# Optimization experiments

Hardware: AMD Instinct MI355X
Metric: run time of the kernel (lower is better)

Reference implementation:

```python
import jax, jax.numpy as jnp
import numpy as np
import math
from jax import lax

N = 5          # kernel_size (hard-coded PHT assumes 5x5)
K = N // 2     # 2
EPS = 1e-6
THETA = 0.7

def _pht_kernel_np():
    # H_i = cos(2*pi*2*r^2 + 0*theta) on the 5x5 grid, times calibrated spectral weights, plus eps
    coords = np.arange(N, dtype=np.float32) - K
    gv, gu = np.meshgrid(coords, coords, indexing='ij')  # torch.meshgrid default is 'ij'
    r2 = (gu ** 2 + gv ** 2) / (K * K + EPS)
    H = np.cos(2.0 * math.pi * 2.0 * r2).astype(np.float32)
    target = np.zeros((N, N), np.float32)
    target[K, K] = -4.0
    target[K - 1, K] = 1.0
    target[K + 1, K] = 1.0
    target[K, K - 1] = 1.0
    target[K, K + 1] = 1.0
    sw = np.where(target != 0, target / H, 0.0).astype(np.float32)
    return (H * sw + EPS).astype(np.float32)  # (5,5)

def _rotation_maps_np():
    # Replicates rotate_kernel exactly: float32 cos/sin, int() truncation, later (h,w) overwrite.
    angles = np.linspace(0, 2 * np.pi, 8, endpoint=False)
    SH = np.zeros((8, N, N), np.int32)
    SW = np.zeros((8, N, N), np.int32)
    M = np.zeros((8, N, N), np.float32)
    for ai, a in enumerate(angles):
        c = float(np.cos(np.float32(a)))
        s = float(np.sin(np.float32(a)))
        for h in range(N):
            for w in range(N):
                rh = int(h * c + w * (-s))
                rw = int(h * s + w * c)
                if 0 <= rh < N and 0 <= rw < N:
                    SH[ai, rh, rw] = h
                    SW[ai, rh, rw] = w
                    M[ai, rh, rw] = 1.0
    return SH, SW, M

_PHT = jnp.asarray(_pht_kernel_np())                     # (5,5)
_sh, _sw, _m = _rotation_maps_np()
_SH = jnp.asarray(_sh)
_SW = jnp.asarray(_sw)
_MASK = jnp.asarray(_m)

def setup_inputs() -> dict:
    key = jax.random.key(0)
    k1, k2 = jax.random.split(key)
    x = jax.random.normal(k1, (32, 64, 128, 128), dtype=jnp.float32)
    weight = jax.random.normal(k2, (64, 64, 5, 5), dtype=jnp.float32) * 0.05
    alpha = jnp.ones((1,), dtype=jnp.float32)
    return {"x": x, "weight": weight, "alpha": alpha}

def reference(x, weight, alpha):
    # Branch 1: PHT-modulated weight, averaged over 8 SO(2) rotations.
    # pht_kernel is (C_in,1,5,5) with identical values per channel -> broadcast (5,5).
    w_eff = weight * alpha[0] * _PHT[None, None]          # (Co,Ci,5,5)
    # rotated[o,i,a,rh,rw] = w_eff[o,i,SH[a,rh,rw],SW[a,rh,rw]] * MASK
    rotated = w_eff[:, :, _SH, _SW] * _MASK               # (Co,Ci,8,5,5)
    # conv is linear in weight: mean of 8 convs == conv with mean kernel
    mean_k = rotated.mean(axis=2)                         # (Co,Ci,5,5)
    out = lax.conv_general_dilated(
        x, mean_k, window_strides=(1, 1), padding=[(2, 2), (2, 2)],
        dimension_numbers=("NCHW", "OIHW", "NCHW"))
    # Branch 2: 1x1 kernel_diff; rotation of a 1x1 kernel is identity, mean of 8 == single conv.
    kd = weight.sum(axis=(2, 3))                          # (Co,Ci)
    out_diff = jnp.einsum("oi,bihw->bohw", kd, x)
    return out - THETA * out_diff
```

## Files before the change

### kernel.cpp

```cpp
#include <hip/hip_runtime.h>
#include <stdint.h>

typedef __attribute__((ext_vector_type(8))) __bf16 bf16x8;
typedef __attribute__((ext_vector_type(16))) float f32x16;
typedef __attribute__((ext_vector_type(4))) unsigned int u32x4;
typedef __attribute__((ext_vector_type(2))) float f32x2;
typedef unsigned int u32;
typedef unsigned short u16;

#define THETA 0.7f

__host__ __device__ constexpr float pht_val(int q) {
  return (q == 12) ? (-4.0f + 1e-6f)
       : (q == 7 || q == 11 || q == 13 || q == 17) ? (1.0f + 1e-6f)
       : 1e-6f;
}

__device__ __forceinline__ u16 f2bf(float v) {
  u32 u = __builtin_bit_cast(u32, v);
  return (u16)((u + 0x7fffu + ((u >> 16) & 1u)) >> 16);
}

__global__ __launch_bounds__(256) void k_prep(const float* __restrict__ wgt,
                                              const float* __restrict__ alpha,
                                              u16* __restrict__ apack) {
  int t = blockIdx.x * 256 + threadIdx.x;
  int o = t >> 6, ci = t & 63;
  const float* wp = wgt + ((size_t)(o * 64 + ci)) * 25;
  float wv[25], sumw = 0.f;
#pragma unroll
  for (int p = 0; p < 25; ++p) { wv[p] = wp[p]; sumw += wv[p]; }
  float keff[25];
#pragma unroll
  for (int p = 0; p < 25; ++p) keff[p] = pht_val(p) * wv[p];
  constexpr int TP[33] = {0,1,2,3,4,6,7,9,12,13,  0,1,2,3,4,  0, 0, 0,
                          0,5,10,15,20,  0,5,6,10,11,12,15,17,20,21};
  constexpr int TQ[33] = {5,6,12,17,23,10,16,22,20,21,  0,5,10,15,20,  5, 0, 5,
                          0,6,7,8,9,  5,6,2,12,8,4,17,9,23,14};
#pragma unroll
  for (int e = 0; e < 33; ++e) keff[TP[e]] += pht_val(TQ[e]) * wv[TQ[e]];

  float al = alpha[0];
  int kc = ci >> 4, oh = o >> 5;
  int lane = ((ci >> 3) & 1) * 32 + (o & 31);
#pragma unroll
  for (int p = 0; p < 25; ++p) {
    float v = al * (keff[p] * 0.125f);
    if (p == 12) v -= THETA * sumw;
    size_t idx = ((((size_t)p * 4 + kc) * 2 + oh) * 64 + lane) * 8 + (ci & 7);
    apack[idx] = f2bf(v);
  }
}

#define ROWB 4608

#define MM(A, B, C) __builtin_amdgcn_mfma_f32_32x32x16_bf16((A), __builtin_bit_cast(bf16x8, (B)), (C), 0, 0, 0)

#define LDBR(S, DX, KC) do {                                                \
    const char* pb_ = pcol + (DX) * 128;                                    \
    int gx_ = ((((KC) * 2 + lhi) ^ ((l31 + (DX)) & 7)) << 4);               \
    br##S##0 = *(const u32x4*)(pb_ + 0 * ROWB + gx_);                       \
    br##S##1 = *(const u32x4*)(pb_ + 1 * ROWB + gx_);                       \
    br##S##2 = *(const u32x4*)(pb_ + 2 * ROWB + gx_);                       \
    br##S##3 = *(const u32x4*)(pb_ + 3 * ROWB + gx_);                       \
    br##S##4 = *(const u32x4*)(pb_ + 4 * ROWB + gx_);                       \
    br##S##5 = *(const u32x4*)(pb_ + 5 * ROWB + gx_);                       \
    br##S##6 = *(const u32x4*)(pb_ + 6 * ROWB + gx_);                       \
    br##S##7 = *(const u32x4*)(pb_ + 7 * ROWB + gx_);                       \
  } while (0)

#define LDAF(S, DX, KC) do {                                                \
    af##S##0 = apb[(size_t)((0 * 5 + (DX)) * 512 + (KC) * 128)];            \
    af##S##1 = apb[(size_t)((1 * 5 + (DX)) * 512 + (KC) * 128)];            \
    af##S##2 = apb[(size_t)((2 * 5 + (DX)) * 512 + (KC) * 128)];            \
    af##S##3 = apb[(size_t)((3 * 5 + (DX)) * 512 + (KC) * 128)];            \
    af##S##4 = apb[(size_t)((4 * 5 + (DX)) * 512 + (KC) * 128)];            \
  } while (0)

#define BURST(S) do {                                                       \
    bf16x8 A_;                                                              \
    A_ = __builtin_bit_cast(bf16x8, af##S##0);                              \
    a0 = MM(A_, br##S##0, a0); a1 = MM(A_, br##S##1, a1);                   \
    a2 = MM(A_, br##S##2, a2); a3 = MM(A_, br##S##3, a3);                   \
    A_ = __builtin_bit_cast(bf16x8, af##S##1);                              \
    a0 = MM(A_, br##S##1, a0); a1 = MM(A_, br##S##2, a1);                   \
    a2 = MM(A_, br##S##3, a2); a3 = MM(A_, br##S##4, a3);                   \
    A_ = __builtin_bit_cast(bf16x8, af##S##2);                              \
    a0 = MM(A_, br##S##2, a0); a1 = MM(A_, br##S##3, a1);                   \
    a2 = MM(A_, br##S##4, a2); a3 = MM(A_, br##S##5, a3);                   \
    A_ = __builtin_bit_cast(bf16x8, af##S##3);                              \
    a0 = MM(A_, br##S##3, a0); a1 = MM(A_, br##S##4, a1);                   \
    a2 = MM(A_, br##S##5, a2); a3 = MM(A_, br##S##6, a3);                   \
    A_ = __builtin_bit_cast(bf16x8, af##S##4);                              \
    a0 = MM(A_, br##S##4, a0); a1 = MM(A_, br##S##5, a1);                   \
    a2 = MM(A_, br##S##6, a2); a3 = MM(A_, br##S##7, a3);                   \
  } while (0)

#define SGB __builtin_amdgcn_sched_group_barrier
#define SCHED_FULL() do {                                                   \
    SGB(0x020, 5, 0);                           \
    SGB(0x100, 2, 0); SGB(0x008, 5, 0);                                     \
    SGB(0x100, 2, 0); SGB(0x008, 5, 0);                                     \
    SGB(0x100, 2, 0); SGB(0x008, 5, 0);                                     \
    SGB(0x100, 2, 0); SGB(0x008, 5, 0);                                     \
  } while (0)

#define ITER(CUR, NXT, DXN, KCN) do {                                       \
    LDBR(NXT, DXN, KCN); LDAF(NXT, DXN, KCN); BURST(CUR); SCHED_FULL();     \
  } while (0)

#define STAGE_SLOT(CP, GG) do {                                             \
    int pxb_ = px0 + 2 * (CP) - 2;                                          \
    bool ok_ = rowok && ((unsigned)pxb_ < 128u);                            \
    const float* ps_ = xr + (size_t)(8 * (GG)) * 16384 + pxb_;              \
    f32x2 v0 = {0.f, 0.f}, v1 = {0.f, 0.f}, v2 = {0.f, 0.f}, v3 = {0.f, 0.f}; \
    f32x2 v4 = {0.f, 0.f}, v5 = {0.f, 0.f}, v6 = {0.f, 0.f}, v7 = {0.f, 0.f}; \
    if (ok_) {                                                              \
      v0 = *(const f32x2*)(ps_);                                            \
      v1 = *(const f32x2*)(ps_ + 16384);                                    \
      v2 = *(const f32x2*)(ps_ + 2 * 16384);                                \
      v3 = *(const f32x2*)(ps_ + 3 * 16384);                                \
      v4 = *(const f32x2*)(ps_ + 4 * 16384);                                \
      v5 = *(const f32x2*)(ps_ + 5 * 16384);                                \
      v6 = *(const f32x2*)(ps_ + 6 * 16384);                                \
      v7 = *(const f32x2*)(ps_ + 7 * 16384);                                \
    }                                                                       \
    u32x4 wx_, wy_;                                                         \
    wx_[0] = (u32)f2bf(v0.x) | ((u32)f2bf(v1.x) << 16);                     \
    wx_[1] = (u32)f2bf(v2.x) | ((u32)f2bf(v3.x) << 16);                     \
    wx_[2] = (u32)f2bf(v4.x) | ((u32)f2bf(v5.x) << 16);                     \
    wx_[3] = (u32)f2bf(v6.x) | ((u32)f2bf(v7.x) << 16);                     \
    wy_[0] = (u32)f2bf(v0.y) | ((u32)f2bf(v1.y) << 16);                     \
    wy_[1] = (u32)f2bf(v2.y) | ((u32)f2bf(v3.y) << 16);                     \
    wy_[2] = (u32)f2bf(v4.y) | ((u32)f2bf(v5.y) << 16);                     \
    wy_[3] = (u32)f2bf(v6.y) | ((u32)f2bf(v7.y) << 16);                     \
    int c0_ = 2 * (CP);                                                     \
    *(u32x4*)(rowbase + c0_ * 128 + (((GG) ^ (c0_ & 7)) << 4)) = wx_;       \
    *(u32x4*)(rowbase + (c0_ + 1) * 128 + (((GG) ^ ((c0_ + 1) & 7)) << 4)) = wy_; \
  } while (0)

__global__ __launch_bounds__(128, 2) void k_conv(const float* __restrict__ x,
                                                 const u32x4* __restrict__ apv,
                                                 float* __restrict__ out) {
  __shared__ char tile[8 * ROWB];
  int bid = blockIdx.x;
  int lg = (bid & 7) * 512 + (bid >> 3);
  int pxq = lg & 3, yt = (lg >> 2) & 31, n = lg >> 7;
  int y0 = yt * 4, px0 = pxq * 32;
  int tid = threadIdx.x;
  int l = tid & 63;

  {
    const float* xn = x + (size_t)n * (64 * 16384);
    int sp = tid & 15, sg = tid >> 4;
    int hp = 16 + (tid >> 3), hg = tid & 7;
#pragma unroll
    for (int rr = 0; rr < 8; ++rr) {
      int sy = y0 + rr - 2;
      bool rowok = (unsigned)sy < 128u;
      char* rowbase = tile + rr * ROWB;
      const float* xr = xn + (size_t)sy * 128;
      STAGE_SLOT(sp, sg);
      if (tid < 16) STAGE_SLOT(hp, hg);
    }
  }

  int oh = tid >> 6;
  int l31 = l & 31, lhi = l >> 5;
  const u32x4* apb = apv + (size_t)(oh * 64 + l);
  const char* pcol = tile + l31 * 128;

  u32x4 brA0, brA1, brA2, brA3, brA4, brA5, brA6, brA7;
  u32x4 brB0, brB1, brB2, brB3, brB4, brB5, brB6, brB7;
  u32x4 afA0, afA1, afA2, afA3, afA4;
  u32x4 afB0, afB1, afB2, afB3, afB4;

  LDAF(A, 0, 0);
  __syncthreads();
  LDBR(A, 0, 0);

  f32x16 a0 = 0, a1 = 0, a2 = 0, a3 = 0;

  ITER(A, B, 0, 1);
  ITER(B, A, 0, 2);
  ITER(A, B, 0, 3);
  ITER(B, A, 1, 0);
  ITER(A, B, 1, 1);
  ITER(B, A, 1, 2);
  ITER(A, B, 1, 3);
  ITER(B, A, 2, 0);
  ITER(A, B, 2, 1);
  ITER(B, A, 2, 2);
  ITER(A, B, 2, 3);
  ITER(B, A, 3, 0);
  ITER(A, B, 3, 1);
  ITER(B, A, 3, 2);
  ITER(A, B, 3, 3);
  ITER(B, A, 4, 0);
  ITER(A, B, 4, 1);
  ITER(B, A, 4, 2);
  ITER(A, B, 4, 3);
  BURST(B);

  float* ob = out + ((size_t)(n * 64 + oh * 32) * 128 + y0) * 128
              + px0 + l31;
#pragma unroll
  for (int rg = 0; rg < 16; ++rg) {
    int orow = (rg & 3) + 8 * (rg >> 2) + 4 * lhi;
    float* obr = ob + (size_t)orow * 16384;
    obr[0]   = a0[rg];
    obr[128] = a1[rg];
    obr[256] = a2[rg];
    obr[384] = a3[rg];
  }
}

extern "C" void kernel_launch(void* const* d_in, const int* in_sizes, int n_in,
                              void* d_out, int out_size, void* d_ws, size_t ws_size,
                              hipStream_t stream) {
  const float* x     = (const float*)d_in[0];
  const float* wgt   = (const float*)d_in[1];
  const float* alpha = (const float*)d_in[2];
  float* out = (float*)d_out;

  u16* apack = (u16*)d_ws;

  k_prep<<<16,   256, 0, stream>>>(wgt, alpha, apack);
  k_conv<<<4096, 128, 0, stream>>>(x, (const u32x4*)apack, out);
}
```

Measured before the change: 131.4 us.

## Process four row tiles per block with a ring buffer and overlapped staging

Each block now computes 16 output rows, in four 4-row steps, instead of 4, so the grid shrinks from 4096 blocks to 1024. A 12-slot ring buffer in LDS holds input rows, and the global loads and bf16 conversion for the next 4 rows are interleaved with the current step's MFMA bursts. This reuses the overlapping halo rows between steps and hides the load latency. Row stride is padded to 4624 bytes. It costs more LDS (about 55KB per block), more registers for the staged values, and fewer blocks, which may hurt occupancy and load balance.

```diff
diff --git a/kernel.cpp b/kernel.cpp
--- a/kernel.cpp
+++ b/kernel.cpp
@@ -52,21 +52,21 @@
   }
 }
 
-#define ROWB 4608
+#define ROWB 4624
+#define NSLOT 12
 
 #define MM(A, B, C) __builtin_amdgcn_mfma_f32_32x32x16_bf16((A), __builtin_bit_cast(bf16x8, (B)), (C), 0, 0, 0)
 
 #define LDBR(S, DX, KC) do {                                                \
-    const char* pb_ = pcol + (DX) * 128;                                    \
     int gx_ = ((((KC) * 2 + lhi) ^ ((l31 + (DX)) & 7)) << 4);               \
-    br##S##0 = *(const u32x4*)(pb_ + 0 * ROWB + gx_);                       \
-    br##S##1 = *(const u32x4*)(pb_ + 1 * ROWB + gx_);                       \
-    br##S##2 = *(const u32x4*)(pb_ + 2 * ROWB + gx_);                       \
-    br##S##3 = *(const u32x4*)(pb_ + 3 * ROWB + gx_);                       \
-    br##S##4 = *(const u32x4*)(pb_ + 4 * ROWB + gx_);                       \
-    br##S##5 = *(const u32x4*)(pb_ + 5 * ROWB + gx_);                       \
-    br##S##6 = *(const u32x4*)(pb_ + 6 * ROWB + gx_);                       \
-    br##S##7 = *(const u32x4*)(pb_ + 7 * ROWB + gx_);                       \
+    br##S##0 = *(const u32x4*)(rb0 + (DX) * 128 + gx_);                     \
+    br##S##1 = *(const u32x4*)(rb1 + (DX) * 128 + gx_);                     \
+    br##S##2 = *(const u32x4*)(rb2 + (DX) * 128 + gx_);                     \
+    br##S##3 = *(const u32x4*)(rb3 + (DX) * 128 + gx_);                     \
+    br##S##4 = *(const u32x4*)(rb4 + (DX) * 128 + gx_);                     \
+    br##S##5 = *(const u32x4*)(rb5 + (DX) * 128 + gx_);                     \
+    br##S##6 = *(const u32x4*)(rb6 + (DX) * 128 + gx_);                     \
+    br##S##7 = *(const u32x4*)(rb7 + (DX) * 128 + gx_);                     \
   } while (0)
 
 #define LDAF(S, DX, KC) do {                                                \
@@ -98,7 +98,7 @@
 
 #define SGB __builtin_amdgcn_sched_group_barrier
 #define SCHED_FULL() do {                                                   \
-    SGB(0x020, 5, 0);                           \
+    SGB(0x020, 5, 0);                                                       \
     SGB(0x100, 2, 0); SGB(0x008, 5, 0);                                     \
     SGB(0x100, 2, 0); SGB(0x008, 5, 0);                                     \
     SGB(0x100, 2, 0); SGB(0x008, 5, 0);                                     \
@@ -109,109 +109,189 @@
     LDBR(NXT, DXN, KCN); LDAF(NXT, DXN, KCN); BURST(CUR); SCHED_FULL();     \
   } while (0)
 
-#define STAGE_SLOT(CP, GG) do {                                             \
-    int pxb_ = px0 + 2 * (CP) - 2;                                          \
-    bool ok_ = rowok && ((unsigned)pxb_ < 128u);                            \
-    const float* ps_ = xr + (size_t)(8 * (GG)) * 16384 + pxb_;              \
-    f32x2 v0 = {0.f, 0.f}, v1 = {0.f, 0.f}, v2 = {0.f, 0.f}, v3 = {0.f, 0.f}; \
-    f32x2 v4 = {0.f, 0.f}, v5 = {0.f, 0.f}, v6 = {0.f, 0.f}, v7 = {0.f, 0.f}; \
-    if (ok_) {                                                              \
-      v0 = *(const f32x2*)(ps_);                                            \
-      v1 = *(const f32x2*)(ps_ + 16384);                                    \
-      v2 = *(const f32x2*)(ps_ + 2 * 16384);                                \
-      v3 = *(const f32x2*)(ps_ + 3 * 16384);                                \
-      v4 = *(const f32x2*)(ps_ + 4 * 16384);                                \
-      v5 = *(const f32x2*)(ps_ + 5 * 16384);                                \
-      v6 = *(const f32x2*)(ps_ + 6 * 16384);                                \
-      v7 = *(const f32x2*)(ps_ + 7 * 16384);                                \
+#define PK(VA, VB) ((u32)f2bf(VA) | ((u32)f2bf(VB) << 16))
+
+#define SLOAD(SYE) do {                                                     \
+    int sy_ = (SYE);                                                        \
+    bool rok_ = (unsigned)sy_ < 128u;                                       \
+    const float* brr_ = xn + (size_t)sy_ * 128;                             \
+    if (rok_ && pxAok) {                                                    \
+      const float* p0_ = brr_ + (size_t)(8 * g0A) * 16384 + pxA;            \
+      const float* p1_ = brr_ + (size_t)(8 * g1A) * 16384 + pxA;            \
+      sv0 = *(const f32x2*)(p0_);               sv1 = *(const f32x2*)(p0_ + 16384);     \
+      sv2 = *(const f32x2*)(p0_ + 2 * 16384);   sv3 = *(const f32x2*)(p0_ + 3 * 16384); \
+      sv4 = *(const f32x2*)(p0_ + 4 * 16384);   sv5 = *(const f32x2*)(p0_ + 5 * 16384); \
+      sv6 = *(const f32x2*)(p0_ + 6 * 16384);   sv7 = *(const f32x2*)(p0_ + 7 * 16384); \
+      sv8 = *(const f32x2*)(p1_);               sv9 = *(const f32x2*)(p1_ + 16384);     \
+      sv10 = *(const f32x2*)(p1_ + 2 * 16384);  sv11 = *(const f32x2*)(p1_ + 3 * 16384);\
+      sv12 = *(const f32x2*)(p1_ + 4 * 16384);  sv13 = *(const f32x2*)(p1_ + 5 * 16384);\
+      sv14 = *(const f32x2*)(p1_ + 6 * 16384);  sv15 = *(const f32x2*)(p1_ + 7 * 16384);\
+    } else {                                                                \
+      sv0 = z2; sv1 = z2; sv2 = z2; sv3 = z2; sv4 = z2; sv5 = z2;           \
+      sv6 = z2; sv7 = z2; sv8 = z2; sv9 = z2; sv10 = z2; sv11 = z2;         \
+      sv12 = z2; sv13 = z2; sv14 = z2; sv15 = z2;                           \
     }                                                                       \
+    if (dutyB) {                                                            \
+      if (rok_ && pxBok) {                                                  \
+        const float* pb_ = brr_ + (size_t)(8 * gB) * 16384 + pxB;           \
+        sb0 = *(const f32x2*)(pb_);              sb1 = *(const f32x2*)(pb_ + 16384);     \
+        sb2 = *(const f32x2*)(pb_ + 2 * 16384);  sb3 = *(const f32x2*)(pb_ + 3 * 16384); \
+        sb4 = *(const f32x2*)(pb_ + 4 * 16384);  sb5 = *(const f32x2*)(pb_ + 5 * 16384); \
+        sb6 = *(const f32x2*)(pb_ + 6 * 16384);  sb7 = *(const f32x2*)(pb_ + 7 * 16384); \
+      } else {                                                              \
+        sb0 = z2; sb1 = z2; sb2 = z2; sb3 = z2;                             \
+        sb4 = z2; sb5 = z2; sb6 = z2; sb7 = z2;                             \
+      }                                                                     \
+    }                                                                       \
+  } while (0)
+
+#define SWRITE(WS) do {                                                     \
+    char* wb_ = tile + (size_t)(WS) * ROWB;                                 \
+    int c0_ = 2 * cpA;                                                      \
     u32x4 wx_, wy_;                                                         \
-    wx_[0] = (u32)f2bf(v0.x) | ((u32)f2bf(v1.x) << 16);                     \
-    wx_[1] = (u32)f2bf(v2.x) | ((u32)f2bf(v3.x) << 16);                     \
-    wx_[2] = (u32)f2bf(v4.x) | ((u32)f2bf(v5.x) << 16);                     \
-    wx_[3] = (u32)f2bf(v6.x) | ((u32)f2bf(v7.x) << 16);                     \
-    wy_[0] = (u32)f2bf(v0.y) | ((u32)f2bf(v1.y) << 16);                     \
-    wy_[1] = (u32)f2bf(v2.y) | ((u32)f2bf(v3.y) << 16);                     \
-    wy_[2] = (u32)f2bf(v4.y) | ((u32)f2bf(v5.y) << 16);                     \
-    wy_[3] = (u32)f2bf(v6.y) | ((u32)f2bf(v7.y) << 16);                     \
-    int c0_ = 2 * (CP);                                                     \
-    *(u32x4*)(rowbase + c0_ * 128 + (((GG) ^ (c0_ & 7)) << 4)) = wx_;       \
-    *(u32x4*)(rowbase + (c0_ + 1) * 128 + (((GG) ^ ((c0_ + 1) & 7)) << 4)) = wy_; \
+    wx_[0] = PK(sv0.x, sv1.x); wx_[1] = PK(sv2.x, sv3.x);                   \
+    wx_[2] = PK(sv4.x, sv5.x); wx_[3] = PK(sv6.x, sv7.x);                   \
+    wy_[0] = PK(sv0.y, sv1.y); wy_[1] = PK(sv2.y, sv3.y);                   \
+    wy_[2] = PK(sv4.y, sv5.y); wy_[3] = PK(sv6.y, sv7.y);                   \
+    *(u32x4*)(wb_ + c0_ * 128 + ((g0A ^ (c0_ & 7)) << 4)) = wx_;            \
+    *(u32x4*)(wb_ + (c0_ + 1) * 128 + ((g0A ^ ((c0_ + 1) & 7)) << 4)) = wy_;\
+    wx_[0] = PK(sv8.x, sv9.x);  wx_[1] = PK(sv10.x, sv11.x);                \
+    wx_[2] = PK(sv12.x, sv13.x); wx_[3] = PK(sv14.x, sv15.x);               \
+    wy_[0] = PK(sv8.y, sv9.y);  wy_[1] = PK(sv10.y, sv11.y);                \
+    wy_[2] = PK(sv12.y, sv13.y); wy_[3] = PK(sv14.y, sv15.y);               \
+    *(u32x4*)(wb_ + c0_ * 128 + ((g1A ^ (c0_ & 7)) << 4)) = wx_;            \
+    *(u32x4*)(wb_ + (c0_ + 1) * 128 + ((g1A ^ ((c0_ + 1) & 7)) << 4)) = wy_;\
+    if (dutyB) {                                                            \
+      int cb_ = 2 * cpB;                                                    \
+      u32x4 ux_, uy_;                                                       \
+      ux_[0] = PK(sb0.x, sb1.x); ux_[1] = PK(sb2.x, sb3.x);                 \
+      ux_[2] = PK(sb4.x, sb5.x); ux_[3] = PK(sb6.x, sb7.x);                 \
+      uy_[0] = PK(sb0.y, sb1.y); uy_[1] = PK(sb2.y, sb3.y);                 \
+      uy_[2] = PK(sb4.y, sb5.y); uy_[3] = PK(sb6.y, sb7.y);                 \
+      *(u32x4*)(wb_ + cb_ * 128 + ((gB ^ (cb_ & 7)) << 4)) = ux_;           \
+      *(u32x4*)(wb_ + (cb_ + 1) * 128 + ((gB ^ ((cb_ + 1) & 7)) << 4)) = uy_;\
+    }                                                                       \
+  } while (0)
+
+#define TBAR() do {                                                         \
+    asm volatile("s_waitcnt lgkmcnt(0)" ::: "memory");                      \
+    __builtin_amdgcn_sched_barrier(0);                                      \
+    __builtin_amdgcn_s_barrier();                                           \
+    __builtin_amdgcn_sched_barrier(0);                                      \
   } while (0)
 
 __global__ __launch_bounds__(128, 2) void k_conv(const float* __restrict__ x,
                                                  const u32x4* __restrict__ apv,
                                                  float* __restrict__ out) {
-  __shared__ char tile[8 * ROWB];
+  __shared__ char tile[NSLOT * ROWB];
   int bid = blockIdx.x;
-  int lg = (bid & 7) * 512 + (bid >> 3);
-  int pxq = lg & 3, yt = (lg >> 2) & 31, n = lg >> 7;
-  int y0 = yt * 4, px0 = pxq * 32;
+  int lg = (bid & 7) * 128 + (bid >> 3);
+  int pxq = lg & 3, yc = (lg >> 2) & 7, n = lg >> 5;
+  int px0 = pxq * 32, yb = yc * 16;
   int tid = threadIdx.x;
-  int l = tid & 63;
-
-  {
-    const float* xn = x + (size_t)n * (64 * 16384);
-    int sp = tid & 15, sg = tid >> 4;
-    int hp = 16 + (tid >> 3), hg = tid & 7;
-#pragma unroll
-    for (int rr = 0; rr < 8; ++rr) {
-      int sy = y0 + rr - 2;
-      bool rowok = (unsigned)sy < 128u;
-      char* rowbase = tile + rr * ROWB;
-      const float* xr = xn + (size_t)sy * 128;
-      STAGE_SLOT(sp, sg);
-      if (tid < 16) STAGE_SLOT(hp, hg);
-    }
-  }
-
-  int oh = tid >> 6;
+  int l = tid & 63, oh = tid >> 6;
   int l31 = l & 31, lhi = l >> 5;
+
+  int rrA = oh;
+  int m = tid & 63;
+  int cpA = m >> 2;
+  int g0A = ((m & 3) * 2 + (cpA & 1)) & 7;
+  int g1A = (g0A + 1) & 7;
+  int pxA = px0 + 2 * cpA - 2;
+  bool pxAok = pxA >= 0;
+  bool dutyB = m < 16;
+  int cpB = 16 + ((m >> 3) & 1);
+  int gB = m & 7;
+  int pxB = px0 + 2 * cpB - 2;
+  bool pxBok = (pxB + 1) < 128;
+
+  const float* xn = x + (size_t)n * (64 * 16384);
+  const f32x2 z2 = {0.f, 0.f};
+
+  f32x2 sv0, sv1, sv2, sv3, sv4, sv5, sv6, sv7;
+  f32x2 sv8, sv9, sv10, sv11, sv12, sv13, sv14, sv15;
+  f32x2 sb0, sb1, sb2, sb3, sb4, sb5, sb6, sb7;
+
+  SLOAD(yb - 2 + 0 + rrA); SWRITE(0 + rrA);
+  SLOAD(yb - 2 + 2 + rrA); SWRITE(2 + rrA);
+  SLOAD(yb - 2 + 4 + rrA); SWRITE(4 + rrA);
+  SLOAD(yb - 2 + 6 + rrA); SWRITE(6 + rrA);
+
   const u32x4* apb = apv + (size_t)(oh * 64 + l);
-  const char* pcol = tile + l31 * 128;
-
   u32x4 brA0, brA1, brA2, brA3, brA4, brA5, brA6, brA7;
   u32x4 brB0, brB1, brB2, brB3, brB4, brB5, brB6, brB7;
   u32x4 afA0, afA1, afA2, afA3, afA4;
   u32x4 afB0, afB1, afB2, afB3, afB4;
 
   LDAF(A, 0, 0);
-  __syncthreads();
-  LDBR(A, 0, 0);
+  TBAR();
 
   f32x16 a0 = 0, a1 = 0, a2 = 0, a3 = 0;
-
-  ITER(A, B, 0, 1);
-  ITER(B, A, 0, 2);
-  ITER(A, B, 0, 3);
-  ITER(B, A, 1, 0);
-  ITER(A, B, 1, 1);
-  ITER(B, A, 1, 2);
-  ITER(A, B, 1, 3);
-  ITER(B, A, 2, 0);
-  ITER(A, B, 2, 1);
-  ITER(B, A, 2, 2);
-  ITER(A, B, 2, 3);
-  ITER(B, A, 3, 0);
-  ITER(A, B, 3, 1);
-  ITER(B, A, 3, 2);
-  ITER(A, B, 3, 3);
-  ITER(B, A, 4, 0);
-  ITER(A, B, 4, 1);
-  ITER(B, A, 4, 2);
-  ITER(A, B, 4, 3);
-  BURST(B);
-
-  float* ob = out + ((size_t)(n * 64 + oh * 32) * 128 + y0) * 128
-              + px0 + l31;
-#pragma unroll
-  for (int rg = 0; rg < 16; ++rg) {
-    int orow = (rg & 3) + 8 * (rg >> 2) + 4 * lhi;
-    float* obr = ob + (size_t)orow * 16384;
-    obr[0]   = a0[rg];
-    obr[128] = a1[rg];
-    obr[256] = a2[rg];
-    obr[384] = a3[rg];
+  char* tl31 = tile + l31 * 128;
+  int b = 0;
+
+#pragma unroll 1
+  for (int t = 0; t < 4; ++t) {
+    int s4 = b + 4; if (s4 >= 12) s4 -= 12;
+    int s5 = b + 5; if (s5 >= 12) s5 -= 12;
+    int s6 = b + 6; if (s6 >= 12) s6 -= 12;
+    int s7 = b + 7; if (s7 >= 12) s7 -= 12;
+    char* rb0 = tl31 + b * ROWB;
+    char* rb1 = tl31 + (b + 1) * ROWB;
+    char* rb2 = tl31 + (b + 2) * ROWB;
+    char* rb3 = tl31 + (b + 3) * ROWB;
+    char* rb4 = tl31 + s4 * ROWB;
+    char* rb5 = tl31 + s5 * ROWB;
+    char* rb6 = tl31 + s6 * ROWB;
+    char* rb7 = tl31 + s7 * ROWB;
+
+    LDBR(A, 0, 0);
+    LDAF(A, 0, 0);
+    ITER(A, B, 0, 1);
+    ITER(B, A, 0, 2);
+    ITER(A, B, 0, 3);
+    ITER(B, A, 1, 0);
+    ITER(A, B, 1, 1);
+    ITER(B, A, 1, 2);
+    if (t < 3) SLOAD(yb + 6 + 4 * t + rrA);
+    ITER(A, B, 1, 3);
+    ITER(B, A, 2, 0);
+    ITER(A, B, 2, 1);
+    if (t < 3) {
+      int wsA = b + 8 + rrA; if (wsA >= 12) wsA -= 12;
+      SWRITE(wsA);
+    }
+    ITER(B, A, 2, 2);
+    ITER(A, B, 2, 3);
+    ITER(B, A, 3, 0);
+    ITER(A, B, 3, 1);
+    ITER(B, A, 3, 2);
+    ITER(A, B, 3, 3);
+    if (t < 3) SLOAD(yb + 8 + 4 * t + rrA);
+    ITER(B, A, 4, 0);
+    ITER(A, B, 4, 1);
+    ITER(B, A, 4, 2);
+    ITER(A, B, 4, 3);
+    BURST(B);
+    if (t < 3) {
+      int wsB = b + 10 + rrA; if (wsB >= 12) wsB -= 12;
+      SWRITE(wsB);
+    }
+
+    float* ob = out + ((size_t)(n * 64 + oh * 32) * 128 + (yb + 4 * t)) * 128
+                + px0 + l31;
+#pragma unroll
+    for (int rg = 0; rg < 16; ++rg) {
+      int orow = (rg & 3) + 8 * (rg >> 2) + 4 * lhi;
+      float* obr = ob + (size_t)orow * 16384;
+      obr[0]   = a0[rg];
+      obr[128] = a1[rg];
+      obr[256] = a2[rg];
+      obr[384] = a3[rg];
+    }
+    a0 = 0; a1 = 0; a2 = 0; a3 = 0;
+    TBAR();
+    b += 4; if (b >= 12) b -= 12;
   }
 }
 
@@ -226,5 +306,5 @@
   u16* apack = (u16*)d_ws;
 
   k_prep<<<16,   256, 0, stream>>>(wgt, alpha, apack);
-  k_conv<<<4096, 128, 0, stream>>>(x, (const u32x4*)apack, out);
-}
+  k_conv<<<1024, 128, 0, stream>>>(x, (const u32x4*)apack, out);
+}
```

After: 202.5 us. +54.1%, slower.
